# Performance work log

Hardware: AMD Instinct MI355X
Metric: run time of the kernel (lower is better)

Reference implementation:

```python
import jax, jax.numpy as jnp
import numpy as np

B, S, H = 2, 2048, 1024
NH, HD = 16, 64


def setup_inputs() -> dict:
    key = jax.random.key(0)
    ks = jax.random.split(key, 6)
    sc = 0.02
    return {
        "hidden_states": jax.random.normal(ks[0], (B, S, H), dtype=jnp.float32),
        "attention_mask": jnp.zeros((B, 1, 1, S), dtype=jnp.float32),
        "rel_pos": jax.random.normal(ks[1], (B, NH, S, S), dtype=jnp.float32) * 0.1,
        "Wq": jax.random.normal(ks[2], (H, H), dtype=jnp.float32) * sc,
        "bq": jnp.zeros((H,), dtype=jnp.float32),
        "Wk": jax.random.normal(ks[3], (H, H), dtype=jnp.float32) * sc,
        "bk": jnp.zeros((H,), dtype=jnp.float32),
        "Wv": jax.random.normal(ks[4], (H, H), dtype=jnp.float32) * sc,
        "bv": jnp.zeros((H,), dtype=jnp.float32),
    }


def reference(hidden_states, attention_mask, rel_pos, Wq, bq, Wk, bk, Wv, bv):
    def heads(x):  # [B,S,H] -> [B,NH,S,HD]
        return x.reshape(B, S, NH, HD).transpose(0, 2, 1, 3)

    q = heads(hidden_states @ Wq.T + bq)
    k = heads(hidden_states @ Wk.T + bk)
    v = heads(hidden_states @ Wv.T + bv)

    scores = jnp.einsum('bhqd,bhkd->bhqk', q, k) / jnp.sqrt(jnp.float32(HD))
    scores = scores + attention_mask + rel_pos
    probs = jax.nn.softmax(scores, axis=-1)
    ctx = jnp.einsum('bhqk,bhkd->bhqd', probs, v)
    return ctx.transpose(0, 2, 1, 3).reshape(B, S, H)
```

## Files before the change

kernel.cpp:

```cpp
#include <hip/hip_runtime.h>
#include <hip/hip_bf16.h>

#define B_  2
#define S_  2048
#define H_  1024
#define NH_ 16
#define HD_ 64

typedef __bf16 bf16_t;
typedef __attribute__((ext_vector_type(4))) __bf16 bf16x4;
typedef __attribute__((ext_vector_type(8))) __bf16 bf16x8;
typedef __attribute__((ext_vector_type(4))) float f32x4;

__device__ __forceinline__ void gld_lds16(const bf16_t* g, bf16_t* l) {
    __builtin_amdgcn_global_load_lds(
        (const __attribute__((address_space(1))) unsigned int*)g,
        (__attribute__((address_space(3))) unsigned int*)l, 16, 0, 0);
}

__global__ __launch_bounds__(256) void cast_bf16(
    const float* __restrict__ X, const float* __restrict__ Wq,
    const float* __restrict__ Wk, const float* __restrict__ Wv,
    bf16_t* __restrict__ Xb, bf16_t* __restrict__ Wb)
{
    const size_t XN = (size_t)B_ * S_ * H_;
    size_t i4 = ((size_t)blockIdx.x * 256 + threadIdx.x) * 4;
    const float* src;
    bf16_t* dst;
    if (i4 < XN) {
        src = X + i4; dst = Xb + i4;
    } else {
        size_t j = i4 - XN;
        int wsel = (int)(j >> 20);
        const float* Wp = wsel == 0 ? Wq : (wsel == 1 ? Wk : Wv);
        src = Wp + (j & 1048575); dst = Wb + j;
    }
    float4 v = *(const float4*)src;
    bf16x4 o = { (bf16_t)v.x, (bf16_t)v.y, (bf16_t)v.z, (bf16_t)v.w };
    *(bf16x4*)dst = o;
}

__global__ __launch_bounds__(256) void qkv_gemm(
    const bf16_t* __restrict__ Xb, const bf16_t* __restrict__ Wb,
    const float* __restrict__ bq, const float* __restrict__ bk,
    const float* __restrict__ bv,
    bf16_t* __restrict__ qbuf, bf16_t* __restrict__ kbuf, bf16_t* __restrict__ vbuf)
{
    const int which = blockIdx.z;
    const bf16_t* W  = Wb + (size_t)which * H_ * H_;
    const float* bias = which == 0 ? bq : (which == 1 ? bk : bv);
    bf16_t* out       = which == 0 ? qbuf : (which == 1 ? kbuf : vbuf);
    const float scale = which == 0 ? 0.125f : 1.0f;

    const int m0 = blockIdx.x * 128;
    const int n0 = blockIdx.y * 128;
    const int t    = threadIdx.x;
    const int lane = t & 63;
    const int w    = t >> 6;
    const int wr   = w >> 1, wc = w & 1;
    const int lo   = lane & 15, g = lane >> 4;

    __shared__ bf16_t As[128 * 64];
    __shared__ bf16_t Bs[128 * 64];

    const int srow = w * 8 + (lane >> 3);
    const int scol = (lane & 7) * 8;
    const bf16_t* ga = Xb + (size_t)(m0 + srow) * H_ + scol;
    const bf16_t* gb = W  + (size_t)(n0 + srow) * H_ + scol;

    f32x4 acc[4][4];
#pragma unroll
    for (int mt = 0; mt < 4; ++mt)
#pragma unroll
        for (int nt = 0; nt < 4; ++nt)
            acc[mt][nt] = (f32x4){0.f, 0.f, 0.f, 0.f};

    for (int kc = 0; kc < 16; ++kc) {
#pragma unroll
        for (int p = 0; p < 4; ++p) {
            gld_lds16(ga + (size_t)p * 32 * H_ + kc * 64, &As[p * 2048 + w * 512]);
            gld_lds16(gb + (size_t)p * 32 * H_ + kc * 64, &Bs[p * 2048 + w * 512]);
        }
        __syncthreads();

        bf16x8 a0[4], a1[4];
#pragma unroll
        for (int mt = 0; mt < 4; ++mt) {
            a0[mt] = *(const bf16x8*)&As[(wr * 64 + mt * 16 + lo) * 64 + g * 8];
            a1[mt] = *(const bf16x8*)&As[(wr * 64 + mt * 16 + lo) * 64 + g * 8 + 32];
        }
#pragma unroll
        for (int nt = 0; nt < 4; ++nt) {
            bf16x8 b0 = *(const bf16x8*)&Bs[(wc * 64 + nt * 16 + lo) * 64 + g * 8];
            bf16x8 b1 = *(const bf16x8*)&Bs[(wc * 64 + nt * 16 + lo) * 64 + g * 8 + 32];
#pragma unroll
            for (int mt = 0; mt < 4; ++mt) {
                acc[mt][nt] = __builtin_amdgcn_mfma_f32_16x16x32_bf16(a0[mt], b0, acc[mt][nt], 0, 0, 0);
                acc[mt][nt] = __builtin_amdgcn_mfma_f32_16x16x32_bf16(a1[mt], b1, acc[mt][nt], 0, 0, 0);
            }
        }
        __syncthreads();
    }

#pragma unroll
    for (int nt = 0; nt < 4; ++nt) {
        int n  = n0 + wc * 64 + nt * 16 + lo;
        int hh = n >> 6, d = n & 63;
        float bv_ = bias[n];
#pragma unroll
        for (int mt = 0; mt < 4; ++mt) {
#pragma unroll
            for (int r = 0; r < 4; ++r) {
                int m = m0 + wr * 64 + mt * 16 + g * 4 + r;
                int b = m >> 11, s = m & 2047;
                out[(((size_t)(b * NH_ + hh) * S_) + s) * HD_ + d] =
                    (bf16_t)((acc[mt][nt][r] + bv_) * scale);
            }
        }
    }
}

__global__ __launch_bounds__(256, 3) void attn(
    const bf16_t* __restrict__ qbuf, const bf16_t* __restrict__ kbuf,
    const bf16_t* __restrict__ vbuf,
    const float* __restrict__ mask, const float* __restrict__ rel,
    float* __restrict__ out)
{
    const int bid  = blockIdx.x;
    const int work = ((bid & 7) << 7) | (bid >> 3);
    const int q0 = (work & 31) * 64;
    const int h  = (work >> 5) & 15;
    const int b  = work >> 9;

    const int t    = threadIdx.x;
    const int lane = t & 63;
    const int w    = t >> 6;
    const int lo   = lane & 15;
    const int g    = lane >> 4;

    __shared__ bf16_t QPs[64 * 72];
    __shared__ bf16_t Ks [64 * 72];
    __shared__ bf16_t VTs[64 * 72];
    __shared__ float  Ms [S_];

    const bf16_t* qg = qbuf + ((size_t)(b * NH_ + h) * S_ + q0) * HD_;
    const bf16_t* kg = kbuf + (size_t)(b * NH_ + h) * S_ * HD_;
    const bf16_t* vg = vbuf + (size_t)(b * NH_ + h) * S_ * HD_;
    const float*  relg  = rel + ((size_t)((b * NH_ + h) * S_ + q0)) * S_;
    const float*  maskg = mask + (size_t)b * S_;

    const int r0 = t >> 3;
    const int c8 = (t & 7) * 8;

    uint4 kv0 = *(const uint4*)&kg[(size_t)r0 * 64 + c8];
    uint4 kv1 = *(const uint4*)&kg[(size_t)(r0 + 32) * 64 + c8];
    uint4 vv0 = *(const uint4*)&vg[(size_t)r0 * 64 + c8];
    uint4 vv1 = *(const uint4*)&vg[(size_t)(r0 + 32) * 64 + c8];

    uint4  qv0 = *(const uint4*)&qg[(size_t)r0 * 64 + c8];
    uint4  qv1 = *(const uint4*)&qg[(size_t)(r0 + 32) * 64 + c8];
    float4 mv0 = *(const float4*)&maskg[t * 8];
    float4 mv1 = *(const float4*)&maskg[t * 8 + 4];

    const int qrow = w * 16 + g * 4;
    float rl[4][4];
#pragma unroll
    for (int r = 0; r < 4; ++r)
#pragma unroll
        for (int nt = 0; nt < 4; ++nt)
            rl[r][nt] = relg[(size_t)(qrow + r) * S_ + nt * 16 + lo];

    *(uint4*)&QPs[r0 * 72 + c8]        = qv0;
    *(uint4*)&QPs[(r0 + 32) * 72 + c8] = qv1;
    *(float4*)&Ms[t * 8]     = mv0;
    *(float4*)&Ms[t * 8 + 4] = mv1;

    asm volatile("s_waitcnt lgkmcnt(0)" ::: "memory");
    __builtin_amdgcn_s_barrier();

    bf16x8 aq0 = *(const bf16x8*)&QPs[(w * 16 + lo) * 72 + g * 8];
    bf16x8 aq1 = *(const bf16x8*)&QPs[(w * 16 + lo) * 72 + g * 8 + 32];

    float mi[4], li[4];
    f32x4 accO[4];
#pragma unroll
    for (int r = 0; r < 4; ++r) { mi[r] = -1e30f; li[r] = 0.f; }
#pragma unroll
    for (int dt = 0; dt < 4; ++dt) accO[dt] = (f32x4){0.f, 0.f, 0.f, 0.f};

    for (int kc = 0; kc < 32; ++kc) {
        *(uint4*)&Ks[r0 * 72 + c8]        = kv0;
        *(uint4*)&Ks[(r0 + 32) * 72 + c8] = kv1;
        {
            const bf16_t* vp0 = (const bf16_t*)&vv0;
            const bf16_t* vp1 = (const bf16_t*)&vv1;
            int sw0 = r0 ^ c8, sw1 = (r0 + 32) ^ c8;
#pragma unroll
            for (int j = 0; j < 8; ++j) {
                VTs[(c8 + j) * 72 + sw0] = vp0[j];
                VTs[(c8 + j) * 72 + sw1] = vp1[j];
            }
        }
        {
            const int kn = (kc < 31) ? kc + 1 : kc;
            const bf16_t* kgn = kg + (size_t)kn * 64 * 64;
            const bf16_t* vgn = vg + (size_t)kn * 64 * 64;
            kv0 = *(const uint4*)&kgn[(size_t)r0 * 64 + c8];
            kv1 = *(const uint4*)&kgn[(size_t)(r0 + 32) * 64 + c8];
            vv0 = *(const uint4*)&vgn[(size_t)r0 * 64 + c8];
            vv1 = *(const uint4*)&vgn[(size_t)(r0 + 32) * 64 + c8];
        }

        asm volatile("s_waitcnt lgkmcnt(0)" ::: "memory");
        __builtin_amdgcn_s_barrier();

        f32x4 sc[4];
        __builtin_amdgcn_s_setprio(1);
#pragma unroll
        for (int nt = 0; nt < 4; ++nt) {
            bf16x8 b0 = *(const bf16x8*)&Ks[(nt * 16 + lo) * 72 + g * 8];
            bf16x8 b1 = *(const bf16x8*)&Ks[(nt * 16 + lo) * 72 + g * 8 + 32];
            f32x4 z = (f32x4){0.f, 0.f, 0.f, 0.f};
            z = __builtin_amdgcn_mfma_f32_16x16x32_bf16(aq0, b0, z, 0, 0, 0);
            z = __builtin_amdgcn_mfma_f32_16x16x32_bf16(aq1, b1, z, 0, 0, 0);
            sc[nt] = z;
        }
        __builtin_amdgcn_s_setprio(0);

        float sv[4][4];
#pragma unroll
        for (int nt = 0; nt < 4; ++nt) {
            float mk = Ms[kc * 64 + nt * 16 + lo];
#pragma unroll
            for (int r = 0; r < 4; ++r)
                sv[r][nt] = sc[nt][r] + mk + rl[r][nt];
        }

        if (kc < 31) {
#pragma unroll
            for (int r = 0; r < 4; ++r)
#pragma unroll
                for (int nt = 0; nt < 4; ++nt)
                    rl[r][nt] = relg[(size_t)(qrow + r) * S_ + (kc + 1) * 64 + nt * 16 + lo];
        }

        bf16_t* Pw = &QPs[w * 16 * 72];
#pragma unroll
        for (int r = 0; r < 4; ++r) {
            float vmax = fmaxf(fmaxf(sv[r][0], sv[r][1]), fmaxf(sv[r][2], sv[r][3]));
#pragma unroll
            for (int mk2 = 1; mk2 < 16; mk2 <<= 1)
                vmax = fmaxf(vmax, __shfl_xor(vmax, mk2, 16));
            float mnew  = fmaxf(mi[r], vmax);
            float alpha = __expf(mi[r] - mnew);
            float rsum = 0.f;
#pragma unroll
            for (int nt = 0; nt < 4; ++nt) {
                float p = __expf(sv[r][nt] - mnew);
                sv[r][nt] = p;
                rsum += p;
            }
#pragma unroll
            for (int mk2 = 1; mk2 < 16; mk2 <<= 1)
                rsum += __shfl_xor(rsum, mk2, 16);
            li[r] = li[r] * alpha + rsum;
            mi[r] = mnew;
#pragma unroll
            for (int dt = 0; dt < 4; ++dt) accO[dt][r] *= alpha;
#pragma unroll
            for (int nt = 0; nt < 4; ++nt)
                Pw[(g * 4 + r) * 72 + ((nt * 16 + lo) ^ (g * 8))] = (bf16_t)sv[r][nt];
        }

        bf16x8 pa0 = *(const bf16x8*)&Pw[lo * 72 + ((g * 8)       ^ ((lo >> 2) * 8))];
        bf16x8 pa1 = *(const bf16x8*)&Pw[lo * 72 + (((4 + g) * 8) ^ ((lo >> 2) * 8))];
        __builtin_amdgcn_s_setprio(1);
#pragma unroll
        for (int dt = 0; dt < 4; ++dt) {
            int d = dt * 16 + lo;
            bf16x8 v0 = *(const bf16x8*)&VTs[d * 72 + ((g * 8)       ^ (d & 56))];
            bf16x8 v1 = *(const bf16x8*)&VTs[d * 72 + (((4 + g) * 8) ^ (d & 56))];
            accO[dt] = __builtin_amdgcn_mfma_f32_16x16x32_bf16(pa0, v0, accO[dt], 0, 0, 0);
            accO[dt] = __builtin_amdgcn_mfma_f32_16x16x32_bf16(pa1, v1, accO[dt], 0, 0, 0);
        }
        __builtin_amdgcn_s_setprio(0);

        __builtin_amdgcn_s_barrier();
    }

#pragma unroll
    for (int dt = 0; dt < 4; ++dt) {
        int d = dt * 16 + lo;
#pragma unroll
        for (int r = 0; r < 4; ++r) {
            int row = q0 + w * 16 + g * 4 + r;
            out[((size_t)(b * S_ + row)) * H_ + h * HD_ + d] = accO[dt][r] / li[r];
        }
    }
}

extern "C" void kernel_launch(void* const* d_in, const int* in_sizes, int n_in,
                              void* d_out, int out_size, void* d_ws, size_t ws_size,
                              hipStream_t stream) {
    const float* hs   = (const float*)d_in[0];
    const float* mask = (const float*)d_in[1];
    const float* rel  = (const float*)d_in[2];
    const float* Wq   = (const float*)d_in[3];
    const float* bq   = (const float*)d_in[4];
    const float* Wk   = (const float*)d_in[5];
    const float* bk   = (const float*)d_in[6];
    const float* Wv   = (const float*)d_in[7];
    const float* bv   = (const float*)d_in[8];
    float* out = (float*)d_out;

    const size_t qkv_elems = (size_t)B_ * NH_ * S_ * HD_;
    bf16_t* qbuf = (bf16_t*)d_ws;
    bf16_t* kbuf = qbuf + qkv_elems;
    bf16_t* vbuf = kbuf + qkv_elems;
    bf16_t* Xb   = vbuf + qkv_elems;
    bf16_t* Wb   = Xb   + qkv_elems;

    cast_bf16<<<7168, 256, 0, stream>>>(hs, Wq, Wk, Wv, Xb, Wb);
    qkv_gemm<<<dim3(32, 8, 3), 256, 0, stream>>>(Xb, Wb, bq, bk, bv,
                                                 qbuf, kbuf, vbuf);
    attn<<<1024, 256, 0, stream>>>(qbuf, kbuf, vbuf, mask, rel, out);
}
```

Measured before the change: 795.7 us.

## Double-buffer QKV GEMM LDS tiles and stage rel_pos through LDS in attention

The QKV GEMM now double-buffers its A/B LDS tiles, prefetching the next K-chunk while computing on the current one, and raises MFMA priority. The attention kernel replaces the scattered per-lane rel_pos loads with coalesced float4 loads that are staged through a double-buffered LDS tile two chunks ahead. The attention occupancy hint drops from 3 to 2 blocks per SM to make room for the extra LDS. The aim is to hide global-load latency, especially on the large rel_pos stream, at the cost of more shared memory and possibly lower occupancy.

```diff
diff --git a/kernel.cpp b/kernel.cpp
--- a/kernel.cpp
+++ b/kernel.cpp
@@ -40,7 +40,7 @@
     *(bf16x4*)dst = o;
 }
 
-__global__ __launch_bounds__(256) void qkv_gemm(
+__global__ __launch_bounds__(256, 2) void qkv_gemm(
     const bf16_t* __restrict__ Xb, const bf16_t* __restrict__ Wb,
     const float* __restrict__ bq, const float* __restrict__ bk,
     const float* __restrict__ bv,
@@ -60,8 +60,8 @@
     const int wr   = w >> 1, wc = w & 1;
     const int lo   = lane & 15, g = lane >> 4;
 
-    __shared__ bf16_t As[128 * 64];
-    __shared__ bf16_t Bs[128 * 64];
+    __shared__ bf16_t As[2][128 * 64];
+    __shared__ bf16_t Bs[2][128 * 64];
 
     const int srow = w * 8 + (lane >> 3);
     const int scol = (lane & 7) * 8;
@@ -75,31 +75,49 @@
         for (int nt = 0; nt < 4; ++nt)
             acc[mt][nt] = (f32x4){0.f, 0.f, 0.f, 0.f};
 
+#pragma unroll
+    for (int p = 0; p < 4; ++p) {
+        gld_lds16(ga + (size_t)p * 32 * H_, &As[0][p * 2048 + w * 512]);
+        gld_lds16(gb + (size_t)p * 32 * H_, &Bs[0][p * 2048 + w * 512]);
+    }
+    asm volatile("s_waitcnt vmcnt(0)" ::: "memory");
+    __builtin_amdgcn_s_barrier();
+
     for (int kc = 0; kc < 16; ++kc) {
-#pragma unroll
-        for (int p = 0; p < 4; ++p) {
-            gld_lds16(ga + (size_t)p * 32 * H_ + kc * 64, &As[p * 2048 + w * 512]);
-            gld_lds16(gb + (size_t)p * 32 * H_ + kc * 64, &Bs[p * 2048 + w * 512]);
-        }
-        __syncthreads();
+        const int cur = kc & 1;
+        if (kc < 15) {
+#pragma unroll
+            for (int p = 0; p < 4; ++p) {
+                gld_lds16(ga + (size_t)p * 32 * H_ + (kc + 1) * 64,
+                          &As[cur ^ 1][p * 2048 + w * 512]);
+                gld_lds16(gb + (size_t)p * 32 * H_ + (kc + 1) * 64,
+                          &Bs[cur ^ 1][p * 2048 + w * 512]);
+            }
+        }
 
         bf16x8 a0[4], a1[4];
 #pragma unroll
         for (int mt = 0; mt < 4; ++mt) {
-            a0[mt] = *(const bf16x8*)&As[(wr * 64 + mt * 16 + lo) * 64 + g * 8];
-            a1[mt] = *(const bf16x8*)&As[(wr * 64 + mt * 16 + lo) * 64 + g * 8 + 32];
-        }
+            a0[mt] = *(const bf16x8*)&As[cur][(wr * 64 + mt * 16 + lo) * 64 + g * 8];
+            a1[mt] = *(const bf16x8*)&As[cur][(wr * 64 + mt * 16 + lo) * 64 + g * 8 + 32];
+        }
+        __builtin_amdgcn_s_setprio(1);
 #pragma unroll
         for (int nt = 0; nt < 4; ++nt) {
-            bf16x8 b0 = *(const bf16x8*)&Bs[(wc * 64 + nt * 16 + lo) * 64 + g * 8];
-            bf16x8 b1 = *(const bf16x8*)&Bs[(wc * 64 + nt * 16 + lo) * 64 + g * 8 + 32];
+            bf16x8 b0 = *(const bf16x8*)&Bs[cur][(wc * 64 + nt * 16 + lo) * 64 + g * 8];
+            bf16x8 b1 = *(const bf16x8*)&Bs[cur][(wc * 64 + nt * 16 + lo) * 64 + g * 8 + 32];
 #pragma unroll
             for (int mt = 0; mt < 4; ++mt) {
                 acc[mt][nt] = __builtin_amdgcn_mfma_f32_16x16x32_bf16(a0[mt], b0, acc[mt][nt], 0, 0, 0);
                 acc[mt][nt] = __builtin_amdgcn_mfma_f32_16x16x32_bf16(a1[mt], b1, acc[mt][nt], 0, 0, 0);
             }
         }
-        __syncthreads();
+        __builtin_amdgcn_s_setprio(0);
+
+        if (kc < 15) {
+            asm volatile("s_waitcnt vmcnt(0)" ::: "memory");
+            __builtin_amdgcn_s_barrier();
+        }
     }
 
 #pragma unroll
@@ -120,7 +138,7 @@
     }
 }
 
-__global__ __launch_bounds__(256, 3) void attn(
+__global__ __launch_bounds__(256, 2) void attn(
     const bf16_t* __restrict__ qbuf, const bf16_t* __restrict__ kbuf,
     const bf16_t* __restrict__ vbuf,
     const float* __restrict__ mask, const float* __restrict__ rel,
@@ -142,6 +160,7 @@
     __shared__ bf16_t Ks [64 * 72];
     __shared__ bf16_t VTs[64 * 72];
     __shared__ float  Ms [S_];
+    __shared__ float  Rs [2][64 * 68];
 
     const bf16_t* qg = qbuf + ((size_t)(b * NH_ + h) * S_ + q0) * HD_;
     const bf16_t* kg = kbuf + (size_t)(b * NH_ + h) * S_ * HD_;
@@ -151,30 +170,36 @@
 
     const int r0 = t >> 3;
     const int c8 = (t & 7) * 8;
+    const int rrow = t >> 2;
+    const int rc16 = (t & 3) * 16;
 
     uint4 kv0 = *(const uint4*)&kg[(size_t)r0 * 64 + c8];
     uint4 kv1 = *(const uint4*)&kg[(size_t)(r0 + 32) * 64 + c8];
     uint4 vv0 = *(const uint4*)&vg[(size_t)r0 * 64 + c8];
     uint4 vv1 = *(const uint4*)&vg[(size_t)(r0 + 32) * 64 + c8];
 
+    float4 rr[4];
+#pragma unroll
+    for (int p = 0; p < 4; ++p)
+        rr[p] = *(const float4*)&relg[(size_t)rrow * S_ + rc16 + p * 4];
+
     uint4  qv0 = *(const uint4*)&qg[(size_t)r0 * 64 + c8];
     uint4  qv1 = *(const uint4*)&qg[(size_t)(r0 + 32) * 64 + c8];
     float4 mv0 = *(const float4*)&maskg[t * 8];
     float4 mv1 = *(const float4*)&maskg[t * 8 + 4];
 
-    const int qrow = w * 16 + g * 4;
-    float rl[4][4];
-#pragma unroll
-    for (int r = 0; r < 4; ++r)
-#pragma unroll
-        for (int nt = 0; nt < 4; ++nt)
-            rl[r][nt] = relg[(size_t)(qrow + r) * S_ + nt * 16 + lo];
-
     *(uint4*)&QPs[r0 * 72 + c8]        = qv0;
     *(uint4*)&QPs[(r0 + 32) * 72 + c8] = qv1;
     *(float4*)&Ms[t * 8]     = mv0;
     *(float4*)&Ms[t * 8 + 4] = mv1;
 
+#pragma unroll
+    for (int p = 0; p < 4; ++p)
+        *(float4*)&Rs[0][rrow * 68 + rc16 + p * 4] = rr[p];
+#pragma unroll
+    for (int p = 0; p < 4; ++p)
+        rr[p] = *(const float4*)&relg[(size_t)rrow * S_ + 64 + rc16 + p * 4];
+
     asm volatile("s_waitcnt lgkmcnt(0)" ::: "memory");
     __builtin_amdgcn_s_barrier();
 
@@ -187,6 +212,8 @@
     for (int r = 0; r < 4; ++r) { mi[r] = -1e30f; li[r] = 0.f; }
 #pragma unroll
     for (int dt = 0; dt < 4; ++dt) accO[dt] = (f32x4){0.f, 0.f, 0.f, 0.f};
+
+    const int qrow = w * 16 + g * 4;
 
     for (int kc = 0; kc < 32; ++kc) {
         *(uint4*)&Ks[r0 * 72 + c8]        = kv0;
@@ -200,6 +227,16 @@
                 VTs[(c8 + j) * 72 + sw0] = vp0[j];
                 VTs[(c8 + j) * 72 + sw1] = vp1[j];
             }
+        }
+        if (kc < 31) {
+            float* Rd = &Rs[(kc + 1) & 1][rrow * 68 + rc16];
+#pragma unroll
+            for (int p = 0; p < 4; ++p)
+                *(float4*)&Rd[p * 4] = rr[p];
+            const int kn = (kc + 2 <= 31) ? kc + 2 : 31;
+#pragma unroll
+            for (int p = 0; p < 4; ++p)
+                rr[p] = *(const float4*)&relg[(size_t)rrow * S_ + kn * 64 + rc16 + p * 4];
         }
         {
             const int kn = (kc < 31) ? kc + 1 : kc;
@@ -227,21 +264,14 @@
         }
         __builtin_amdgcn_s_setprio(0);
 
+        const float* Rc = &Rs[kc & 1][0];
         float sv[4][4];
 #pragma unroll
         for (int nt = 0; nt < 4; ++nt) {
             float mk = Ms[kc * 64 + nt * 16 + lo];
 #pragma unroll
             for (int r = 0; r < 4; ++r)
-                sv[r][nt] = sc[nt][r] + mk + rl[r][nt];
-        }
-
-        if (kc < 31) {
-#pragma unroll
-            for (int r = 0; r < 4; ++r)
-#pragma unroll
-                for (int nt = 0; nt < 4; ++nt)
-                    rl[r][nt] = relg[(size_t)(qrow + r) * S_ + (kc + 1) * 64 + nt * 16 + lo];
+                sv[r][nt] = sc[nt][r] + mk + Rc[(qrow + r) * 68 + nt * 16 + lo];
         }
 
         bf16_t* Pw = &QPs[w * 16 * 72];
@@ -285,6 +315,7 @@
         }
         __builtin_amdgcn_s_setprio(0);
 
+        asm volatile("s_waitcnt lgkmcnt(0)" ::: "memory");
         __builtin_amdgcn_s_barrier();
     }
 
```

Measured after the change: 885.4 us. +11.3%, slower.
